# Optimization experiments

Measured on AMD Instinct MI355X. Metric: run time of the kernel, lower is better.

## Reference

```python
import jax, jax.numpy as jnp
import numpy as np

B, T, D_IN, D_OUT = 4, 2048, 1024, 1024


def setup_inputs() -> dict:
    key = jax.random.key(0)
    k1, k2, k3, k4 = jax.random.split(key, 4)
    s = 0.02  # keep activations in a sane range
    x = jax.random.normal(k1, (B, T, D_IN), dtype=jnp.float32)
    Wq = jax.random.normal(k2, (D_IN, D_OUT), dtype=jnp.float32) * s
    Wk = jax.random.normal(k3, (D_IN, D_OUT), dtype=jnp.float32) * s
    Wv = jax.random.normal(k4, (D_IN, D_OUT), dtype=jnp.float32) * s
    return {"x": x, "Wq": Wq, "Wk": Wk, "Wv": Wv}


def reference(x, Wq, Wk, Wv):
    # Linear projections (torch Linear: y = x @ W^T, here W stored as [d_in, d_out])
    q = jnp.einsum('btd,de->bte', x, Wq)
    k = jnp.einsum('btd,de,->bte', x, Wk, jnp.float32(1.0)) if False else jnp.einsum('btd,de->bte', x, Wk)
    v = jnp.einsum('btd,de->bte', x, Wv)
    # Full [B, T, T] score matrix (faithful to the hand-rolled implementation)
    scores = jnp.einsum('bqe,bke->bqk', q, k)
    T_ = x.shape[1]
    causal = jnp.triu(jnp.ones((T_, T_), dtype=bool), k=1)  # True above diagonal
    scores = jnp.where(causal[None, :, :], -jnp.inf, scores)
    scale = 1.0 / jnp.sqrt(jnp.asarray(k.shape[-1], dtype=scores.dtype))
    attn = jax.nn.softmax(scores * scale, axis=-1)
    # dropout p=0.0 -> identity
    return jnp.einsum('bqk,bke->bqe', attn, v)
```

## Files before the change

### kernel.cpp

```cpp
#include <hip/hip_runtime.h>
#include <hip/hip_bf16.h>
#include <cstdint>

typedef __attribute__((ext_vector_type(8))) short short8;
typedef __attribute__((ext_vector_type(4))) short short4v;
typedef __attribute__((ext_vector_type(4))) float floatx4;
typedef unsigned short ushort;

__device__ __forceinline__ float bf2f(ushort u) {
  unsigned int x = ((unsigned int)u) << 16;
  return __builtin_bit_cast(float, x);
}
__device__ __forceinline__ ushort f2bf(float f) {
  unsigned int x = __builtin_bit_cast(unsigned int, f);
  x += 0x7fffu + ((x >> 16) & 1u);
  return (ushort)(x >> 16);
}

__device__ __forceinline__ void gload_lds16(const void* g, void* l) {
  __builtin_amdgcn_global_load_lds(
      (const __attribute__((address_space(1))) void*)g,
      (__attribute__((address_space(3))) void*)l, 16, 0, 0);
}


__global__ __launch_bounds__(256) void prep_kernel(const float* __restrict__ x,
                                                   const float* __restrict__ Wq,
                                                   const float* __restrict__ Wk,
                                                   const float* __restrict__ Wv,
                                                   ushort* __restrict__ xb,
                                                   ushort* __restrict__ Wt) {
  int bid = blockIdx.x;
  int tid = threadIdx.x;
  if (bid < 4096) {
    int i = bid * 256 + tid;
    const float4* xf = (const float4*)x;
    float4 a = xf[i * 2], b = xf[i * 2 + 1];
    short8 o;
    o[0] = (short)f2bf(a.x); o[1] = (short)f2bf(a.y);
    o[2] = (short)f2bf(a.z); o[3] = (short)f2bf(a.w);
    o[4] = (short)f2bf(b.x); o[5] = (short)f2bf(b.y);
    o[6] = (short)f2bf(b.z); o[7] = (short)f2bf(b.w);
    ((short8*)xb)[i] = o;
  } else {
    int t = bid - 4096;
    int z = t >> 8;
    int rem = t & 255;
    int c0 = (rem & 15) * 64;
    int r0 = (rem >> 4) * 64;
    const float* W = z == 0 ? Wq : (z == 1 ? Wk : Wv);
    ushort* O = Wt + (size_t)z * 1024 * 1024;
    __shared__ float tile[64][65];
#pragma unroll
    for (int i = 0; i < 4; ++i) {
      int c = tid + i * 256; int rr = c >> 4, q = c & 15;
      float4 v = *(const float4*)&W[(size_t)(r0 + rr) * 1024 + c0 + q * 4];
      tile[rr][q * 4 + 0] = v.x; tile[rr][q * 4 + 1] = v.y;
      tile[rr][q * 4 + 2] = v.z; tile[rr][q * 4 + 3] = v.w;
    }
    __syncthreads();
#pragma unroll
    for (int i = 0; i < 2; ++i) {
      int c = tid + i * 256; int oc = c >> 3, q = c & 7;
      short8 o;
#pragma unroll
      for (int j = 0; j < 8; ++j) o[j] = (short)f2bf(tile[q * 8 + j][oc]);
      *(short8*)&O[(size_t)(c0 + oc) * 1024 + r0 + q * 8] = o;
    }
  }
}


__global__ __launch_bounds__(512, 2) void qkv8_kernel(const ushort* __restrict__ A,
                                                      const ushort* __restrict__ Bm,
                                                      ushort* __restrict__ Qo,
                                                      ushort* __restrict__ Ko,
                                                      ushort* __restrict__ Vt) {
  __shared__ __align__(16) ushort lds[2][2][2][8192];

  const int tid = threadIdx.x;
  const int lane = tid & 63;
  const int wave = tid >> 6;
  const int wm = wave >> 2;
  const int wn = wave & 3;
  const int r15 = lane & 15;
  const int kg = lane >> 4;

  const int nwgx = 32, nwgy = 12;
  int orig = blockIdx.y * nwgx + blockIdx.x;
  int swz = (orig & 7) * ((nwgx * nwgy) >> 3) + (orig >> 3);
  int by = swz % nwgy;
  int bx = swz / nwgy;
  const int m0 = bx * 256;
  const int n0 = by * 256;

  const ushort* Ag = A + (size_t)m0 * 1024;
  const ushort* Bg = Bm + (size_t)n0 * 1024;

  const int NKT = 16;

  floatx4 acc[8][4] = {};

  auto stage = [&](int sidx) {
    int kt = sidx >> 2, hh = sidx & 3;
    int mat = hh & 1, kh = hh >> 1;
    ushort* dst = &lds[kt & 1][mat][kh][0];
    const ushort* src = mat ? Bg : Ag;
    int kbase = kt * 64 + kh * 32;
#pragma unroll
    for (int i = 0; i < 2; ++i) {
      int t = tid + i * 512;
      int d = t * 16;
      int L = d ^ (((d >> 7) & 3) << 4);
      int row = L >> 6;
      int colE = (L & 63) >> 1;
      gload_lds16(src + (size_t)row * 1024 + kbase + colE, dst + t * 8);
    }
  };

  auto ldA = [&](int buf, int ks, int m) -> short8 {
    int row = wm * 128 + m * 16 + r15;
    int L = row * 64 + kg * 16;
    int P = L ^ (((row >> 1) & 3) << 4);
    return *(const short8*)((const char*)&lds[buf][0][ks][0] + P);
  };
  auto ldB = [&](int buf, int ks, int n) -> short8 {
    int row = wn * 64 + n * 16 + r15;
    int L = row * 64 + kg * 16;
    int P = L ^ (((row >> 1) & 3) << 4);
    return *(const short8*)((const char*)&lds[buf][1][ks][0] + P);
  };

  for (int s = 0; s < 6; ++s) stage(s);
  asm volatile("s_waitcnt vmcnt(8)" ::: "memory");
  __builtin_amdgcn_s_barrier();

  short8 bfrag[4];
  int sidx = 6;
  for (int kt = 0; kt < NKT; ++kt) {
    int cur = kt & 1;
#pragma unroll
    for (int q = 0; q < 4; ++q) {
      const int ks = q >> 1;
      const int msub = (q & 1) * 4;
      short8 afrag[4];
      if ((q & 1) == 0) {
#pragma unroll
        for (int n = 0; n < 4; ++n) bfrag[n] = ldB(cur, ks, n);
      }
#pragma unroll
      for (int m = 0; m < 4; ++m) afrag[m] = ldA(cur, ks, msub + m);
      if (sidx < NKT * 4) stage(sidx);
      ++sidx;
      if (q & 1) asm volatile("s_waitcnt vmcnt(4)" ::: "memory");
      __builtin_amdgcn_s_barrier();
      asm volatile("s_waitcnt lgkmcnt(0)" ::: "memory");
      __builtin_amdgcn_sched_barrier(0);
      __builtin_amdgcn_s_setprio(1);
#pragma unroll
      for (int m = 0; m < 4; ++m)
#pragma unroll
        for (int n = 0; n < 4; ++n)
          acc[msub + m][n] =
              __builtin_amdgcn_mfma_f32_16x16x32_bf16(afrag[m], bfrag[n], acc[msub + m][n], 0, 0, 0);
      __builtin_amdgcn_s_setprio(0);
      __builtin_amdgcn_s_barrier();
    }
  }

  const int z = n0 >> 10;
  const int rq = kg * 4;
  if (z < 2) {
    ushort* Cz = z == 0 ? Qo : Ko;
    const int cb = n0 & 1023;
#pragma unroll
    for (int m = 0; m < 8; ++m) {
#pragma unroll
      for (int n = 0; n < 4; ++n) {
        int gc = cb + wn * 64 + n * 16 + r15;
#pragma unroll
        for (int r = 0; r < 4; ++r) {
          int gr = m0 + wm * 128 + m * 16 + rq + r;
          Cz[(size_t)gr * 1024 + gc] = f2bf(acc[m][n][r]);
        }
      }
    }
  } else {
#pragma unroll
    for (int m = 0; m < 8; ++m) {
      int gr = m0 + wm * 128 + m * 16 + rq;
      int b = gr >> 11;
      int t = gr & 2047;
      ushort* Vb = Vt + (size_t)b * 1024 * 2048;
#pragma unroll
      for (int n = 0; n < 4; ++n) {
        int e = (n0 - 2048) + wn * 64 + n * 16 + r15;
        short4v o;
#pragma unroll
        for (int r = 0; r < 4; ++r) o[r] = (short)f2bf(acc[m][n][r]);
        *(short4v*)&Vb[(size_t)e * 2048 + t] = o;
      }
    }
  }
}


__global__ __launch_bounds__(256) void s_kernel(const ushort* __restrict__ Q,
                                                const ushort* __restrict__ K,
                                                ushort* __restrict__ S,
                                                float* __restrict__ Lpart) {
  int t = blockIdx.x;
  int qb = (int)((sqrtf(8.f * (float)t + 1.f) - 1.f) * 0.5f);
  while ((qb + 1) * (qb + 2) / 2 <= t) ++qb;
  while (qb * (qb + 1) / 2 > t) --qb;
  int kb = t - qb * (qb + 1) / 2;
  const size_t bi = blockIdx.y;
  const ushort* Ag = Q + bi * 2048 * 1024 + (size_t)qb * 128 * 1024;
  const ushort* Bg = K + bi * 2048 * 1024 + (size_t)kb * 128 * 1024;
  ushort* C = S + bi * 2048 * 2048;
  const int m0 = qb * 128, n0 = kb * 128;

  __shared__ __align__(16) ushort Asm[2][128 * 32];
  __shared__ __align__(16) ushort Bsm[2][128 * 32];
  __shared__ float rsum_lds[4][64];
  const int tid = threadIdx.x;
  const int lane = tid & 63;
  const int wave = tid >> 6;
  const int wrow = (wave >> 1) * 64;
  const int wcol = (wave & 1) * 64;
  const int r15 = lane & 15;
  const int kg = (lane >> 4) * 8;

  floatx4 acc[4][4] = {};

  auto stage = [&](int buf, int kt) {
    int k0 = kt * 32;
#pragma unroll
    for (int i = 0; i < 2; ++i) {
      int c = tid + i * 256;
      gload_lds16(Ag + (size_t)(c >> 2) * 1024 + k0 + (c & 3) * 8, &Asm[buf][c * 8]);
    }
#pragma unroll
    for (int i = 0; i < 2; ++i) {
      int c = tid + i * 256;
      gload_lds16(Bg + (size_t)(c >> 2) * 1024 + k0 + (c & 3) * 8, &Bsm[buf][c * 8]);
    }
  };

  stage(0, 0);
  for (int kt = 0; kt < 32; ++kt) {
    int cur = kt & 1;
    __syncthreads();
    if (kt + 1 < 32) stage(cur ^ 1, kt + 1);
    short8 af[4], bfr[4];
#pragma unroll
    for (int m = 0; m < 4; ++m)
      af[m] = *(const short8*)&Asm[cur][(wrow + m * 16 + r15) * 32 + kg];
#pragma unroll
    for (int n = 0; n < 4; ++n)
      bfr[n] = *(const short8*)&Bsm[cur][(wcol + n * 16 + r15) * 32 + kg];
#pragma unroll
    for (int m = 0; m < 4; ++m)
#pragma unroll
      for (int n = 0; n < 4; ++n)
        acc[m][n] = __builtin_amdgcn_mfma_f32_16x16x32_bf16(af[m], bfr[n], acc[m][n], 0, 0, 0);
  }

  const int rq = (lane >> 4) * 4;
  const float K2 = 0.03125f * 1.44269504f;
#pragma unroll
  for (int m = 0; m < 4; ++m) {
    float rs[4] = {0.f, 0.f, 0.f, 0.f};
#pragma unroll
    for (int n = 0; n < 4; ++n) {
      int gc = n0 + wcol + n * 16 + r15;
#pragma unroll
      for (int r = 0; r < 4; ++r) {
        int gr = m0 + wrow + m * 16 + rq + r;
        float ev = (gc <= gr) ? __builtin_amdgcn_exp2f(acc[m][n][r] * K2) : 0.f;
        C[(size_t)gr * 2048 + gc] = f2bf(ev);
        rs[r] += ev;
      }
    }
#pragma unroll
    for (int r = 0; r < 4; ++r) {
#pragma unroll
      for (int off = 1; off < 16; off <<= 1) rs[r] += __shfl_xor(rs[r], off, 64);
    }
    if (r15 == 0) {
#pragma unroll
      for (int r = 0; r < 4; ++r) rsum_lds[wave][m * 16 + rq + r] = rs[r];
    }
  }
  __syncthreads();
  if (tid < 128) {
    int h = tid >> 6;
    int lr = tid & 63;
    float v = rsum_lds[h * 2][lr] + rsum_lds[h * 2 + 1][lr];
    Lpart[((size_t)bi * 16 + kb) * 2048 + m0 + h * 64 + lr] = v;
  }
}


__global__ __launch_bounds__(256) void lred_kernel(const float* __restrict__ Lpart,
                                                   float* __restrict__ Lp) {
  int row = blockIdx.x * 256 + threadIdx.x;
  int b = row >> 11, r = row & 2047;
  int qb = r >> 7;
  float s = 0.f;
  for (int kb = 0; kb <= qb; ++kb) s += Lpart[((size_t)b * 16 + kb) * 2048 + r];
  Lp[row] = 1.f / s;
}


__global__ __launch_bounds__(256) void pv_kernel(const ushort* __restrict__ E,
                                                 const ushort* __restrict__ Vt,
                                                 const float* __restrict__ Lp,
                                                 float* __restrict__ O) {
  const int qb = 15 - blockIdx.x;
  const int nb = blockIdx.y;
  const size_t bi = blockIdx.z;
  const int kTiles = (qb + 1) * 4;
  const ushort* Ag = E + bi * 2048 * 2048 + (size_t)qb * 128 * 2048;
  const ushort* Bg = Vt + bi * 1024 * 2048 + (size_t)nb * 128 * 2048;
  float* Ob = O + bi * 2048 * 1024;
  const int m0 = qb * 128, n0 = nb * 128;

  __shared__ __align__(16) ushort Asm[2][128 * 32];
  __shared__ __align__(16) ushort Bsm[2][128 * 32];
  const int tid = threadIdx.x;
  const int lane = tid & 63;
  const int wave = tid >> 6;
  const int wrow = (wave >> 1) * 64;
  const int wcol = (wave & 1) * 64;
  const int r15 = lane & 15;
  const int kg = (lane >> 4) * 8;

  floatx4 acc[4][4] = {};

  auto stage = [&](int buf, int kt) {
    int k0 = kt * 32;
#pragma unroll
    for (int i = 0; i < 2; ++i) {
      int c = tid + i * 256;
      gload_lds16(Ag + (size_t)(c >> 2) * 2048 + k0 + (c & 3) * 8, &Asm[buf][c * 8]);
    }
#pragma unroll
    for (int i = 0; i < 2; ++i) {
      int c = tid + i * 256;
      gload_lds16(Bg + (size_t)(c >> 2) * 2048 + k0 + (c & 3) * 8, &Bsm[buf][c * 8]);
    }
  };

  stage(0, 0);
  for (int kt = 0; kt < kTiles; ++kt) {
    int cur = kt & 1;
    __syncthreads();
    if (kt + 1 < kTiles) stage(cur ^ 1, kt + 1);
    short8 af[4], bfr[4];
#pragma unroll
    for (int m = 0; m < 4; ++m)
      af[m] = *(const short8*)&Asm[cur][(wrow + m * 16 + r15) * 32 + kg];
#pragma unroll
    for (int n = 0; n < 4; ++n)
      bfr[n] = *(const short8*)&Bsm[cur][(wcol + n * 16 + r15) * 32 + kg];
#pragma unroll
    for (int m = 0; m < 4; ++m)
#pragma unroll
      for (int n = 0; n < 4; ++n)
        acc[m][n] = __builtin_amdgcn_mfma_f32_16x16x32_bf16(af[m], bfr[n], acc[m][n], 0, 0, 0);
  }

  const int rq = (lane >> 4) * 4;
#pragma unroll
  for (int m = 0; m < 4; ++m) {
#pragma unroll
    for (int r = 0; r < 4; ++r) {
      int gr = m0 + wrow + m * 16 + rq + r;
      float il = Lp[bi * 2048 + gr];
#pragma unroll
      for (int n = 0; n < 4; ++n) {
        int gc = n0 + wcol + n * 16 + r15;
        Ob[(size_t)gr * 1024 + gc] = acc[m][n][r] * il;
      }
    }
  }
}


extern "C" void kernel_launch(void* const* d_in, const int* in_sizes, int n_in,
                              void* d_out, int out_size, void* d_ws, size_t ws_size,
                              hipStream_t stream) {
  const float* x  = (const float*)d_in[0];
  const float* Wq = (const float*)d_in[1];
  const float* Wk = (const float*)d_in[2];
  const float* Wv = (const float*)d_in[3];
  float* out = (float*)d_out;

  ushort* Xb  = (ushort*)d_ws;
  ushort* Wt  = Xb + (size_t)8192 * 1024;
  ushort* QK  = Wt + (size_t)3 * 1024 * 1024;
  ushort* Vt  = QK + (size_t)2 * 8192 * 1024;
  ushort* S   = Vt + (size_t)4 * 1024 * 2048;
  float*  Lpart = (float*)(S + (size_t)4 * 2048 * 2048);
  float*  Lp    = Lpart + (size_t)4 * 16 * 2048;

  ushort* Qp = QK;
  ushort* Kp = QK + (size_t)8192 * 1024;

  hipLaunchKernelGGL(prep_kernel, dim3(4864), dim3(256), 0, stream, x, Wq, Wk, Wv, Xb, Wt);
  hipLaunchKernelGGL(qkv8_kernel, dim3(32, 12), dim3(512), 0, stream, Xb, Wt, Qp, Kp, Vt);
  hipLaunchKernelGGL(s_kernel, dim3(136, 4), dim3(256), 0, stream, Qp, Kp, S, Lpart);
  hipLaunchKernelGGL(lred_kernel, dim3(32), dim3(256), 0, stream, Lpart, Lp);
  hipLaunchKernelGGL(pv_kernel, dim3(16, 8, 4), dim3(256), 0, stream, S, Vt, Lp, out);
}
```

Measured before the change: 178.1 us.

## Widen QKV GEMM tile to 256x384 with triple-buffered K=32 pipeline

The fused QKV projection GEMM moves from 256x256 tiles (384 workgroups) to 256x384 tiles (256 workgroups, one per CU on the 256-CU part). The K loop now runs in 32-wide steps with three LDS buffers instead of 64-wide double buffering. The aim is to give each workgroup more MFMA work per loaded A fragment, so each A load is reused across 6 B tiles instead of 4, and to avoid a partial wave of workgroups. In exchange it needs more accumulator registers (8x6 floatx4) and more LDS, which may reduce occupancy or cause spills, and each epilogue tile now mixes Q, K and V output.

```diff
diff --git a/kernel.cpp b/kernel.cpp
--- a/kernel.cpp
+++ b/kernel.cpp
@@ -71,12 +71,13 @@
 }
 
 
-__global__ __launch_bounds__(512, 2) void qkv8_kernel(const ushort* __restrict__ A,
-                                                      const ushort* __restrict__ Bm,
-                                                      ushort* __restrict__ Qo,
-                                                      ushort* __restrict__ Ko,
-                                                      ushort* __restrict__ Vt) {
-  __shared__ __align__(16) ushort lds[2][2][2][8192];
+__global__ __launch_bounds__(512, 2) void qkv_kernel(const ushort* __restrict__ A,
+                                                     const ushort* __restrict__ Bm,
+                                                     ushort* __restrict__ Qo,
+                                                     ushort* __restrict__ Ko,
+                                                     ushort* __restrict__ Vt) {
+  __shared__ __align__(16) ushort ldsA[3][8192];
+  __shared__ __align__(16) ushort ldsB[3][12288];
 
   const int tid = threadIdx.x;
   const int lane = tid & 63;
@@ -86,119 +87,118 @@
   const int r15 = lane & 15;
   const int kg = lane >> 4;
 
-  const int nwgx = 32, nwgy = 12;
-  int orig = blockIdx.y * nwgx + blockIdx.x;
-  int swz = (orig & 7) * ((nwgx * nwgy) >> 3) + (orig >> 3);
-  int by = swz % nwgy;
-  int bx = swz / nwgy;
-  const int m0 = bx * 256;
-  const int n0 = by * 256;
+  int orig = blockIdx.y * 32 + blockIdx.x;
+  int swz = (orig & 7) * 32 + (orig >> 3);
+  const int m0 = (swz >> 3) * 256;
+  const int n0 = (swz & 7) * 384;
 
   const ushort* Ag = A + (size_t)m0 * 1024;
   const ushort* Bg = Bm + (size_t)n0 * 1024;
 
-  const int NKT = 16;
-
-  floatx4 acc[8][4] = {};
-
-  auto stage = [&](int sidx) {
-    int kt = sidx >> 2, hh = sidx & 3;
-    int mat = hh & 1, kh = hh >> 1;
-    ushort* dst = &lds[kt & 1][mat][kh][0];
-    const ushort* src = mat ? Bg : Ag;
-    int kbase = kt * 64 + kh * 32;
-#pragma unroll
-    for (int i = 0; i < 2; ++i) {
-      int t = tid + i * 512;
-      int d = t * 16;
+  const int NKT = 32;
+
+  floatx4 acc[8][6] = {};
+
+  auto stageA = [&](int kt) {
+    ushort* dst = &ldsA[kt % 3][0];
+    int k0 = kt * 32;
+#pragma unroll
+    for (int i = 0; i < 2; ++i) {
+      int s = wave * 128 + i * 64 + lane;
+      int d = s * 16;
       int L = d ^ (((d >> 7) & 3) << 4);
-      int row = L >> 6;
-      int colE = (L & 63) >> 1;
-      gload_lds16(src + (size_t)row * 1024 + kbase + colE, dst + t * 8);
-    }
-  };
-
-  auto ldA = [&](int buf, int ks, int m) -> short8 {
+      gload_lds16(Ag + (size_t)(L >> 6) * 1024 + k0 + ((L & 63) >> 1), dst + s * 8);
+    }
+  };
+  auto stageB = [&](int kt) {
+    ushort* dst = &ldsB[kt % 3][0];
+    int k0 = kt * 32;
+#pragma unroll
+    for (int i = 0; i < 3; ++i) {
+      int s = wave * 192 + i * 64 + lane;
+      int d = s * 16;
+      int L = d ^ (((d >> 7) & 3) << 4);
+      gload_lds16(Bg + (size_t)(L >> 6) * 1024 + k0 + ((L & 63) >> 1), dst + s * 8);
+    }
+  };
+
+  auto ldA = [&](int buf, int m) -> short8 {
     int row = wm * 128 + m * 16 + r15;
-    int L = row * 64 + kg * 16;
-    int P = L ^ (((row >> 1) & 3) << 4);
-    return *(const short8*)((const char*)&lds[buf][0][ks][0] + P);
-  };
-  auto ldB = [&](int buf, int ks, int n) -> short8 {
-    int row = wn * 64 + n * 16 + r15;
-    int L = row * 64 + kg * 16;
-    int P = L ^ (((row >> 1) & 3) << 4);
-    return *(const short8*)((const char*)&lds[buf][1][ks][0] + P);
-  };
-
-  for (int s = 0; s < 6; ++s) stage(s);
-  asm volatile("s_waitcnt vmcnt(8)" ::: "memory");
+    int P = (row * 64 + kg * 16) ^ (((row >> 1) & 3) << 4);
+    return *(const short8*)((const char*)&ldsA[buf][0] + P);
+  };
+  auto ldB = [&](int buf, int n) -> short8 {
+    int row = wn * 96 + n * 16 + r15;
+    int P = (row * 64 + kg * 16) ^ (((row >> 1) & 3) << 4);
+    return *(const short8*)((const char*)&ldsB[buf][0] + P);
+  };
+
+  stageA(0); stageB(0); stageA(1); stageB(1);
+  asm volatile("s_waitcnt vmcnt(5)" ::: "memory");
   __builtin_amdgcn_s_barrier();
 
-  short8 bfrag[4];
-  int sidx = 6;
+  short8 bfrag[6], afrag[4];
   for (int kt = 0; kt < NKT; ++kt) {
-    int cur = kt & 1;
-#pragma unroll
-    for (int q = 0; q < 4; ++q) {
-      const int ks = q >> 1;
-      const int msub = (q & 1) * 4;
-      short8 afrag[4];
-      if ((q & 1) == 0) {
-#pragma unroll
-        for (int n = 0; n < 4; ++n) bfrag[n] = ldB(cur, ks, n);
-      }
-#pragma unroll
-      for (int m = 0; m < 4; ++m) afrag[m] = ldA(cur, ks, msub + m);
-      if (sidx < NKT * 4) stage(sidx);
-      ++sidx;
-      if (q & 1) asm volatile("s_waitcnt vmcnt(4)" ::: "memory");
-      __builtin_amdgcn_s_barrier();
-      asm volatile("s_waitcnt lgkmcnt(0)" ::: "memory");
-      __builtin_amdgcn_sched_barrier(0);
-      __builtin_amdgcn_s_setprio(1);
-#pragma unroll
-      for (int m = 0; m < 4; ++m)
-#pragma unroll
-        for (int n = 0; n < 4; ++n)
-          acc[msub + m][n] =
-              __builtin_amdgcn_mfma_f32_16x16x32_bf16(afrag[m], bfrag[n], acc[msub + m][n], 0, 0, 0);
-      __builtin_amdgcn_s_setprio(0);
-      __builtin_amdgcn_s_barrier();
-    }
-  }
-
-  const int z = n0 >> 10;
+    const int buf = kt % 3;
+
+#pragma unroll
+    for (int n = 0; n < 6; ++n) bfrag[n] = ldB(buf, n);
+#pragma unroll
+    for (int m = 0; m < 4; ++m) afrag[m] = ldA(buf, m);
+    if (kt + 2 < NKT) stageA(kt + 2);
+    __builtin_amdgcn_s_barrier();
+    asm volatile("s_waitcnt lgkmcnt(0)" ::: "memory");
+    __builtin_amdgcn_sched_barrier(0);
+    __builtin_amdgcn_s_setprio(1);
+#pragma unroll
+    for (int m = 0; m < 4; ++m)
+#pragma unroll
+      for (int n = 0; n < 6; ++n)
+        acc[m][n] = __builtin_amdgcn_mfma_f32_16x16x32_bf16(afrag[m], bfrag[n], acc[m][n], 0, 0, 0);
+    __builtin_amdgcn_s_setprio(0);
+    __builtin_amdgcn_s_barrier();
+
+#pragma unroll
+    for (int m = 0; m < 4; ++m) afrag[m] = ldA(buf, m + 4);
+    if (kt + 2 < NKT) stageB(kt + 2);
+    if (kt < NKT - 2)
+      asm volatile("s_waitcnt vmcnt(5)" ::: "memory");
+    else if (kt == NKT - 2)
+      asm volatile("s_waitcnt vmcnt(0)" ::: "memory");
+    __builtin_amdgcn_s_barrier();
+    asm volatile("s_waitcnt lgkmcnt(0)" ::: "memory");
+    __builtin_amdgcn_sched_barrier(0);
+    __builtin_amdgcn_s_setprio(1);
+#pragma unroll
+    for (int m = 0; m < 4; ++m)
+#pragma unroll
+      for (int n = 0; n < 6; ++n)
+        acc[m + 4][n] = __builtin_amdgcn_mfma_f32_16x16x32_bf16(afrag[m], bfrag[n], acc[m + 4][n], 0, 0, 0);
+    __builtin_amdgcn_s_setprio(0);
+    __builtin_amdgcn_s_barrier();
+  }
+
   const int rq = kg * 4;
-  if (z < 2) {
-    ushort* Cz = z == 0 ? Qo : Ko;
-    const int cb = n0 & 1023;
-#pragma unroll
-    for (int m = 0; m < 8; ++m) {
-#pragma unroll
-      for (int n = 0; n < 4; ++n) {
-        int gc = cb + wn * 64 + n * 16 + r15;
-#pragma unroll
-        for (int r = 0; r < 4; ++r) {
-          int gr = m0 + wm * 128 + m * 16 + rq + r;
-          Cz[(size_t)gr * 1024 + gc] = f2bf(acc[m][n][r]);
-        }
-      }
-    }
-  } else {
-#pragma unroll
-    for (int m = 0; m < 8; ++m) {
-      int gr = m0 + wm * 128 + m * 16 + rq;
-      int b = gr >> 11;
-      int t = gr & 2047;
-      ushort* Vb = Vt + (size_t)b * 1024 * 2048;
-#pragma unroll
-      for (int n = 0; n < 4; ++n) {
-        int e = (n0 - 2048) + wn * 64 + n * 16 + r15;
+#pragma unroll
+  for (int m = 0; m < 8; ++m) {
+    int grb = m0 + wm * 128 + m * 16 + rq;
+#pragma unroll
+    for (int n = 0; n < 6; ++n) {
+      int gc0 = n0 + wn * 96 + n * 16;
+      if (gc0 < 2048) {
+        ushort* Cz = gc0 < 1024 ? Qo : Ko;
+        int col = (gc0 & 1023) + r15;
+#pragma unroll
+        for (int r = 0; r < 4; ++r)
+          Cz[(size_t)(grb + r) * 1024 + col] = f2bf(acc[m][n][r]);
+      } else {
+        int e = gc0 - 2048 + r15;
+        int b = grb >> 11;
+        int t = grb & 2047;
         short4v o;
 #pragma unroll
         for (int r = 0; r < 4; ++r) o[r] = (short)f2bf(acc[m][n][r]);
-        *(short4v*)&Vb[(size_t)e * 2048 + t] = o;
+        *(short4v*)&Vt[((size_t)b * 1024 + e) * 2048 + t] = o;
       }
     }
   }
@@ -409,7 +409,7 @@
   ushort* Kp = QK + (size_t)8192 * 1024;
 
   hipLaunchKernelGGL(prep_kernel, dim3(4864), dim3(256), 0, stream, x, Wq, Wk, Wv, Xb, Wt);
-  hipLaunchKernelGGL(qkv8_kernel, dim3(32, 12), dim3(512), 0, stream, Xb, Wt, Qp, Kp, Vt);
+  hipLaunchKernelGGL(qkv_kernel, dim3(32, 8), dim3(512), 0, stream, Xb, Wt, Qp, Kp, Vt);
   hipLaunchKernelGGL(s_kernel, dim3(136, 4), dim3(256), 0, stream, Qp, Kp, S, Lpart);
   hipLaunchKernelGGL(lred_kernel, dim3(32), dim3(256), 0, stream, Lpart, Lp);
   hipLaunchKernelGGL(pv_kernel, dim3(16, 8, 4), dim3(256), 0, stream, S, Vt, Lp, out);
```

Result: slower. 189.3 us (+6.3%).
